# Performance work log

Hardware: AMD Instinct MI355X
Metric: run time of the kernel (lower is better)

Reference implementation:

```python
import jax, jax.numpy as jnp
import numpy as np

NUM_SPHERICAL = 7
NUM_RADIAL = 6
CUTOFF = 5.0
ENV_EXPONENT = 5
N_EDGES = 500000
N_TRIPLETS = 2000000


def _sph_jn_np(x, n):
    # spherical Bessel j_n(x) via upward recurrence (numpy, used for zero finding)
    j0 = np.sin(x) / x
    if n == 0:
        return j0
    j1 = np.sin(x) / x ** 2 - np.cos(x) / x
    jm1, j = j0, j1
    for l in range(1, n):
        jm1, j = j, (2 * l + 1) / x * j - jm1
    return j


def _jn_zeros(n, k):
    # zeros of spherical Bessel j_l, l=0..n-1, first k each (interlacing + bisection)
    def bisect(f, a, b):
        fa = f(a)
        for _ in range(80):
            m = 0.5 * (a + b)
            fm = f(m)
            if fa * fm <= 0:
                b = m
            else:
                a, fa = m, fm
        return 0.5 * (a + b)

    zerosj = np.zeros((n, k))
    zerosj[0] = np.arange(1, k + 1) * np.pi
    points = np.arange(1, k + n) * np.pi
    for i in range(1, n):
        m = k + n - 1 - i
        racines = np.zeros(m)
        for j in range(m):
            racines[j] = bisect(lambda r: _sph_jn_np(r, i), points[j], points[j + 1])
        points = racines
        zerosj[i] = racines[:k]
    return zerosj


_Z = _jn_zeros(NUM_SPHERICAL, NUM_RADIAL)  # [L, R] Bessel zeros
_BNORM = np.array([[1.0 / np.sqrt(0.5 * _sph_jn_np(_Z[l, n], l + 1) ** 2)
                    for n in range(NUM_RADIAL)] for l in range(NUM_SPHERICAL)])  # [L, R]
_YNORM = np.array([np.sqrt((2 * l + 1) / (4 * np.pi)) for l in range(NUM_SPHERICAL)])


def _sph_jn(x, n):
    # jnp spherical Bessel j_n via upward recurrence; x > 0 guaranteed here
    j0 = jnp.sin(x) / x
    if n == 0:
        return j0
    j1 = jnp.sin(x) / x ** 2 - jnp.cos(x) / x
    jm1, j = j0, j1
    for l in range(1, n):
        jm1, j = j, (2 * l + 1) / x * j - jm1
    return j


def setup_inputs() -> dict:
    key = jax.random.key(0)
    k1, k2, k3, k4 = jax.random.split(key, 4)
    D_ca = jax.random.uniform(k1, (N_EDGES,), dtype=jnp.float32) * (0.99 * CUTOFF) + 0.01
    Angle_cab = jax.random.uniform(k2, (N_TRIPLETS,), dtype=jnp.float32) * np.pi
    id3_reduce_ca = jax.random.randint(k3, (N_TRIPLETS,), 0, N_EDGES, dtype=jnp.int32)
    Kidx = jax.random.randint(k4, (N_TRIPLETS,), 0, 64, dtype=jnp.int32)
    return {"D_ca": D_ca, "Angle_cab": Angle_cab,
            "id3_reduce_ca": id3_reduce_ca, "Kidx": Kidx}


def reference(D_ca, Angle_cab, id3_reduce_ca, Kidx):
    L, R = NUM_SPHERICAL, NUM_RADIAL
    inv_cutoff = 1.0 / CUTOFF
    d = D_ca * inv_cutoff  # [E]

    # envelope u(d) = 1/d + a d^{p-1} + b d^p + c d^{p+1}, zero for d >= 1
    p = ENV_EXPONENT + 1
    a = -(p + 1) * (p + 2) / 2.0
    b = float(p * (p + 2))
    c = -p * (p + 1) / 2.0
    env = 1.0 / d + a * d ** (p - 1) + b * d ** p + c * d ** (p + 1)
    u_d = jnp.where(d < 1.0, env, jnp.zeros_like(d))

    zf = jnp.asarray(_Z, dtype=d.dtype)      # [L, R]
    bn = jnp.asarray(_BNORM, dtype=d.dtype)  # [L, R]
    # radial basis: norm_{l,n} * j_l(z_{l,n} * d)   -> [E, L, R]
    rbf = jnp.stack([bn[l] * _sph_jn(d[:, None] * zf[l], l) for l in range(L)], axis=1)
    norm_const = inv_cutoff ** 1.5
    rbf_env = (u_d * norm_const)[:, None, None] * rbf  # [E, L, R]

    # angular basis: Y_l^0(theta) = sqrt((2l+1)/4pi) * P_l(cos theta)  -> [T, L]
    ct = jnp.cos(Angle_cab)
    P = [jnp.ones_like(ct), ct]
    for l in range(1, L - 1):
        P.append(((2 * l + 1) * ct * P[l] - l * P[l - 1]) / (l + 1))
    yn = jnp.asarray(_YNORM, dtype=ct.dtype)
    sph = jnp.stack([yn[l] * P[l] for l in range(L)], axis=1)  # [T, L]

    # gather per-edge radial features to triplets and modulate by angular part
    out = rbf_env[id3_reduce_ca] * sph[:, :, None]  # [T, L, R]
    return out.reshape(-1, L * R)
```

## Files before the change

### kernel.cpp

```cpp
#include <hip/hip_runtime.h>
#include <math.h>
#include <stdint.h>

#define NSPH 7
#define NRAD 6
#define BLK  256
#define EPB  6
#define NE_PAD 48

typedef float f32x2 __attribute__((ext_vector_type(2)));
typedef float f32x4 __attribute__((ext_vector_type(4)));

#define SC_HPI_INV 0x1.45F306DC9C883p+23
#define SC_HPI     0x1.921FB54442D18p+0
#define SC_C0      (0x1p+0)
#define SC_C1      (-0x1.ffffffd0c621cp-2)
#define SC_C2      (0x1.55553e1068f19p-5)
#define SC_C3      (-0x1.6c087e89a359dp-10)
#define SC_C4      (0x1.99343027bf8c3p-16)
#define SC_S1      (-0x1.555545995a603p-3)
#define SC_S2      (0x1.1107605230bc4p-7)
#define SC_S3      (-0x1.994eb3774cf24p-13)

__device__ __forceinline__ unsigned abstop12(float x) {
    return (__float_as_uint(x) >> 20) & 0x7ffu;
}

__device__ __forceinline__ float sp_sin(double x, double x2) {
    double x3 = __dmul_rn(x, x2);
    double s1 = __dadd_rn(SC_S2, __dmul_rn(x2, SC_S3));
    double x7 = __dmul_rn(x3, x2);
    double s  = __dadd_rn(x, __dmul_rn(x3, SC_S1));
    return (float)__dadd_rn(s, __dmul_rn(x7, s1));
}

__device__ __forceinline__ float sp_cos(double x2, bool neg) {
    double c0 = neg ? -SC_C0 : SC_C0;
    double c1 = neg ? -SC_C1 : SC_C1;
    double c2 = neg ? -SC_C2 : SC_C2;
    double c3 = neg ? -SC_C3 : SC_C3;
    double c4 = neg ? -SC_C4 : SC_C4;
    double x4  = __dmul_rn(x2, x2);
    double c2v = __dadd_rn(c3, __dmul_rn(x2, c4));
    double c1v = __dadd_rn(c0, __dmul_rn(x2, c1));
    double x6  = __dmul_rn(x4, x2);
    double c   = __dadd_rn(c1v, __dmul_rn(x4, c2));
    return (float)__dadd_rn(c, __dmul_rn(x6, c2v));
}

__device__ __forceinline__ float sp_cos_pos(double x2) {
    double x4  = __dmul_rn(x2, x2);
    double c2v = __dadd_rn(SC_C3, __dmul_rn(x2, SC_C4));
    double c1v = __dadd_rn(SC_C0, __dmul_rn(x2, SC_C1));
    double x6  = __dmul_rn(x4, x2);
    double c   = __dadd_rn(c1v, __dmul_rn(x4, SC_C2));
    return (float)__dadd_rn(c, __dmul_rn(x6, c2v));
}

__device__ __forceinline__ double reduce_fast(double x, int* np) {
    double r = __dmul_rn(x, SC_HPI_INV);
    int n = (((int)r) + 0x800000) >> 24;
    *np = n;
    return __dsub_rn(x, __dmul_rn((double)n, SC_HPI));
}

__device__ __forceinline__ float glibc_cosf(float y) {
    unsigned at = abstop12(y);
    double x = (double)y;
    if (at < 0x3f4u) {
        if (at < 0x398u) return 1.0f;
        return sp_cos(__dmul_rn(x, x), false);
    }
    int n;
    double r = reduce_fast(x, &n);
    double s = ((n + 2) & 2) ? -1.0 : 1.0;
    bool neg = ((n + 1) & 2) != 0;
    int m = n ^ 1;
    double xs = __dmul_rn(r, s);
    double x2 = __dmul_rn(r, r);
    if ((m & 1) == 0) return sp_sin(xs, x2);
    return sp_cos(x2, neg);
}

__device__ __forceinline__ void glibc_sincosf(float y, float& so, float& co) {
    unsigned at = abstop12(y);
    double x = (double)y;
    if (at < 0x3f4u) {
        if (at < 0x398u) { so = y; co = 1.0f; return; }
        double x2 = __dmul_rn(x, x);
        so = sp_sin(x, x2);
        co = sp_cos(x2, false);
        return;
    }
    int n;
    double r = reduce_fast(x, &n);
    double x2 = __dmul_rn(r, r);
    double ss = ((n + 1) & 2) ? -1.0 : 1.0;
    double cs = ((n + 2) & 2) ? -1.0 : 1.0;
    bool sneg = (n & 2) != 0;
    bool cneg = ((n + 1) & 2) != 0;
    if ((n & 1) == 0) {
        so = sp_sin(__dmul_rn(r, ss), x2);
        co = sp_cos(x2, cneg);
    } else {
        so = sp_cos(x2, sneg);
        co = sp_sin(__dmul_rn(r, cs), x2);
    }
}

__device__ __forceinline__ void sincos_nr(float y, float& so, float& co) {
    int n;
    double r = reduce_fast((double)y, &n);
    double x2 = __dmul_rn(r, r);
    float sps = sp_sin(r, x2);
    float spc = sp_cos_pos(x2);
    unsigned sbit = (unsigned)(n & 2) << 30;
    unsigned cbit = (unsigned)((n + 1) & 2) << 30;
    bool odd = (n & 1) != 0;
    float sv = odd ? spc : sps;
    float cv = odd ? sps : spc;
    so = __uint_as_float(__float_as_uint(sv) ^ sbit);
    co = __uint_as_float(__float_as_uint(cv) ^ cbit);
}

__device__ __forceinline__ double jn_f64(double x, int n) {
    double s = sin(x), c = cos(x);
    double j0 = s / x;
    if (n == 0) return j0;
    double j1 = s / (x * x) - c / x;
    double jm1 = j0, j = j1;
    for (int l = 1; l < n; ++l) {
        double t = (double)(2 * l + 1) / x * j - jm1;
        jm1 = j; j = t;
    }
    return j;
}

__global__ __launch_bounds__(704) void setup_k(float* __restrict__ cst) {
    __shared__ double pts[13];
    __shared__ double roots[12];
    __shared__ double Z[NSPH][NRAD];
    const double PI = 3.141592653589793238462643383279502884;
    int tid = threadIdx.x, wv = tid >> 6, ln = tid & 63;
    if (tid < 12) pts[tid] = PI * (double)(tid + 1);
    __syncthreads();
    if (tid < NRAD) Z[0][tid] = pts[tid];
    for (int i = 1; i < NSPH; ++i) {
        int m = NRAD + NSPH - 1 - i;
        if (wv < m) {
            double a = pts[wv], b = pts[wv + 1];
            for (int r = 0; r < 9; ++r) {
                double st = (b - a) * (1.0 / 63.0);
                double f = jn_f64(a + st * (double)ln, i);
                double f0 = __shfl(f, 0);
                unsigned long long bm = __ballot((ln > 0) && (f0 * f <= 0.0));
                int idx = bm ? (__ffsll((unsigned long long)bm) - 1) : 63;
                b = a + st * (double)idx;
                a = a + st * (double)(idx - 1);
            }
            if (ln == 0) roots[wv] = 0.5 * (a + b);
        }
        __syncthreads();
        if (tid < m) pts[tid] = roots[tid];
        if (tid < NRAD) Z[i][tid] = roots[tid];
        __syncthreads();
    }
    if (tid < NSPH * NRAD) {
        int l = tid / NRAD;
        double z = Z[l][tid % NRAD];
        cst[tid] = (float)z;
        double jp = jn_f64(z, l + 1);
        cst[42 + tid] = (float)(1.0 / sqrt(0.5 * (jp * jp)));
    }
    if (tid < NSPH) {
        cst[84 + tid] = (float)sqrt((double)(2 * tid + 1) / (4.0 * PI));
    }
}

__global__ __launch_bounds__(252) void edge_k(
    const float* __restrict__ D, const float* __restrict__ cst,
    float* __restrict__ tab, int nE)
{
    __shared__ float zf[42], bn[42];
    __shared__ float sh_d[EPB], sh_unc[EPB];
    int tid = threadIdx.x;
    if (tid < 42) { zf[tid] = cst[tid]; bn[tid] = cst[42 + tid]; }
    int l   = tid / 36;
    int rem = tid - l * 36;
    int le  = rem / 6;
    int n   = rem - le * 6;
    int k   = l * 6 + n;
    long long e = (long long)blockIdx.x * EPB + le;
    bool ok = e < (long long)nE;
    if (ok && k == 0) {
        float d = __fmul_rn(D[e], 0.2f);
        float invd = __fdiv_rn(1.0f, d);
        float d2 = d * d, d4 = d2 * d2, d5 = d4 * d, d6 = d5 * d, d7 = d6 * d;
        float env = ((invd + (-28.0f) * d5) + 48.0f * d6) + (-21.0f) * d7;
        float u_d = (d < 1.0f) ? env : 0.0f;
        const float NC = (float)0.0894427190999916;
        sh_unc[le] = __fmul_rn(u_d, NC);
        sh_d[le] = d;
    }
    __syncthreads();
    if (!ok) return;
    float d = sh_d[le], unc = sh_unc[le];

    float x = __fmul_rn(d, zf[k]);
    float s, c;
    sincos_nr(x, s, c);
    float j = __fdiv_rn(s, x);
    if (l > 0) {
        float x2 = __fmul_rn(x, x);
        float j1 = __fsub_rn(__fdiv_rn(s, x2), __fdiv_rn(c, x));
        float jm1 = j, jc = j1;
        for (int kk = 1; kk < l; ++kk) {
            float fk = __fdiv_rn((float)(2 * kk + 1), x);
            float jn2 = __fsub_rn(__fmul_rn(fk, jc), jm1);
            jm1 = jc; jc = jn2;
        }
        j = jc;
    }
    tab[e * NE_PAD + k] = __fmul_rn(unc, __fmul_rn(bn[k], j));
}

__global__ __launch_bounds__(BLK) void trip_k(
    const float* __restrict__ Ang, const int* __restrict__ id3,
    const float* __restrict__ tab, const float* __restrict__ cst,
    float* __restrict__ out, int nT)
{
    __shared__ int   esh[BLK];
    __shared__ float ysh[BLK * 8];
    int tid = threadIdx.x;
    int base = blockIdx.x * BLK;
    int t = base + tid;
    bool ok = t < nT;
    int e = ok ? __builtin_nontemporal_load(id3 + t) : 0;
    float ang = ok ? __builtin_nontemporal_load(Ang + t) : 0.0f;
    esh[tid] = e * 24;

    float ct = glibc_cosf(ang);
    float P[NSPH];
    P[0] = 1.0f; P[1] = ct;
#pragma unroll
    for (int l = 1; l < NSPH - 1; ++l) {
        float t1 = __fmul_rn(__fmul_rn((float)(2 * l + 1), ct), P[l]);
        float t2 = __fmul_rn((float)l, P[l - 1]);
        P[l + 1] = __fdiv_rn(__fsub_rn(t1, t2), (float)(l + 1));
    }
#pragma unroll
    for (int l = 0; l < NSPH; ++l)
        ysh[tid * 8 + l] = __fmul_rn(cst[84 + l], P[l]);
    __syncthreads();

    const f32x2* tab2 = (const f32x2*)tab;
    f32x2* dst = (f32x2*)out + (long long)base * 21;
    int nv = nT - base; if (nv > BLK) nv = BLK;
    if (nv == BLK) {
#pragma unroll
        for (int it = 0; it < 21; ++it) {
            int i = tid + it * BLK;
            int r = i / 21, p = i - r * 21;
            f32x2 v = tab2[esh[r] + p];
            float ym = ysh[r * 8 + p / 3];
            f32x2 w;
            w.x = __fmul_rn(v.x, ym);
            w.y = __fmul_rn(v.y, ym);
            __builtin_nontemporal_store(w, dst + i);
        }
    } else {
        int nf2 = nv * 21; if (nf2 < 0) nf2 = 0;
        for (int i = tid; i < nf2; i += BLK) {
            int r = i / 21, p = i - r * 21;
            f32x2 v = tab2[esh[r] + p];
            float ym = ysh[r * 8 + p / 3];
            f32x2 w;
            w.x = __fmul_rn(v.x, ym);
            w.y = __fmul_rn(v.y, ym);
            __builtin_nontemporal_store(w, dst + i);
        }
    }
}

__global__ __launch_bounds__(BLK) void sph_main(
    const float* __restrict__ D, const float* __restrict__ Ang,
    const int* __restrict__ id3, const float* __restrict__ cst,
    float* __restrict__ out, int nT)
{
    __shared__ float zf[42], bn[42], yn[7];
    __shared__ float stg[BLK * 42];
    int tid = threadIdx.x;
    if (tid < 42) { zf[tid] = cst[tid]; bn[tid] = cst[42 + tid]; }
    if (tid < 7)  { yn[tid] = cst[84 + tid]; }
    __syncthreads();
    int base = blockIdx.x * BLK;
    int t = base + tid;
    bool ok = t < nT;
    int e = ok ? id3[t] : 0;
    float Dv = D[e];
    float ang = ok ? Ang[t] : 0.0f;
    float d = __fmul_rn(Dv, 0.2f);
    float invd = __fdiv_rn(1.0f, d);
    float d2 = d * d, d4 = d2 * d2, d5 = d4 * d, d6 = d5 * d, d7 = d6 * d;
    float env = ((invd + (-28.0f) * d5) + 48.0f * d6) + (-21.0f) * d7;
    float u_d = (d < 1.0f) ? env : 0.0f;
    const float NC = (float)0.0894427190999916;
    float unc = __fmul_rn(u_d, NC);
    float ct = glibc_cosf(ang);
    float P[NSPH];
    P[0] = 1.0f; P[1] = ct;
#pragma unroll
    for (int l = 1; l < NSPH - 1; ++l) {
        float t1 = __fmul_rn(__fmul_rn((float)(2 * l + 1), ct), P[l]);
        float t2 = __fmul_rn((float)l, P[l - 1]);
        P[l + 1] = __fdiv_rn(__fsub_rn(t1, t2), (float)(l + 1));
    }
    float* row = &stg[tid * 42];
#pragma unroll
    for (int l = 0; l < NSPH; ++l) {
        float yPl = __fmul_rn(yn[l], P[l]);
        for (int n = 0; n < NRAD; ++n) {
            float z = zf[l * 6 + n];
            float x = __fmul_rn(d, z);
            float s, c;
            glibc_sincosf(x, s, c);
            float j = __fdiv_rn(s, x);
            if (l > 0) {
                float x2 = __fmul_rn(x, x);
                float j1 = __fsub_rn(__fdiv_rn(s, x2), __fdiv_rn(c, x));
                float jm1 = j, jc = j1;
                for (int kk = 1; kk < l; ++kk) {
                    float fk = __fdiv_rn((float)(2 * kk + 1), x);
                    float jn2 = __fsub_rn(__fmul_rn(fk, jc), jm1);
                    jm1 = jc; jc = jn2;
                }
                j = jc;
            }
            float re = __fmul_rn(unc, __fmul_rn(bn[l * 6 + n], j));
            row[l * 6 + n] = __fmul_rn(re, yPl);
        }
    }
    __syncthreads();
    int nv = nT - base; if (nv > BLK) nv = BLK;
    int nf2 = nv * 21;
    const float2* src = (const float2*)stg;
    float2* dst = (float2*)(out + (long long)base * 42);
    for (int i = tid; i < nf2; i += BLK) dst[i] = src[i];
}

extern "C" void kernel_launch(void* const* d_in, const int* in_sizes, int n_in,
                              void* d_out, int out_size, void* d_ws, size_t ws_size,
                              hipStream_t stream) {
    const float* D   = (const float*)d_in[0];
    const float* Ang = (const float*)d_in[1];
    const int*   id3 = (const int*)d_in[2];
    float* out = (float*)d_out;
    int nE = in_sizes[0];
    int nT = in_sizes[1];

    size_t tab_bytes = (size_t)nE * NE_PAD * sizeof(float);
    if (ws_size >= tab_bytes + 512) {
        float* tab = (float*)d_ws;
        float* cst = (float*)((char*)d_ws + tab_bytes);
        setup_k<<<1, 704, 0, stream>>>(cst);
        int gA = (nE + EPB - 1) / EPB;
        edge_k<<<gA, 252, 0, stream>>>(D, cst, tab, nE);
        int gB = (nT + BLK - 1) / BLK;
        trip_k<<<gB, BLK, 0, stream>>>(Ang, id3, tab, cst, out, nT);
    } else {
        float* cst = (float*)d_ws;
        setup_k<<<1, 704, 0, stream>>>(cst);
        int grid = (nT + BLK - 1) / BLK;
        sph_main<<<grid, BLK, 0, stream>>>(D, Ang, id3, cst, out, nT);
    }
}
```

Before: 264.6 us.

## Split envelope into separate kernel and remap edge_k threads per wavefront by l

The envelope computation moves out of edge_k into a new env_k kernel that writes the per-edge scale into padding slot 47 of the table, which removes the shared-memory staging and the __syncthreads in edge_k. edge_k now uses 448-thread blocks with one 64-lane wavefront per spherical order l, so each wavefront runs the same Bessel recurrence length and divergence drops. The cost is an extra kernel launch, an extra table read per thread, and 4 idle lanes per wavefront.

```diff
diff --git a/kernel.cpp b/kernel.cpp
--- a/kernel.cpp
+++ b/kernel.cpp
@@ -5,7 +5,7 @@
 #define NSPH 7
 #define NRAD 6
 #define BLK  256
-#define EPB  6
+#define EPB2 10
 #define NE_PAD 48
 
 typedef float f32x2 __attribute__((ext_vector_type(2)));
@@ -177,36 +177,39 @@
     }
 }
 
-__global__ __launch_bounds__(252) void edge_k(
+__global__ __launch_bounds__(BLK) void env_k(
+    const float* __restrict__ D, float* __restrict__ tab, int nE)
+{
+    int e = blockIdx.x * BLK + threadIdx.x;
+    if (e >= nE) return;
+    float d = __fmul_rn(D[e], 0.2f);
+    float invd = __fdiv_rn(1.0f, d);
+    float d2 = d * d, d4 = d2 * d2, d5 = d4 * d, d6 = d5 * d, d7 = d6 * d;
+    float env = ((invd + (-28.0f) * d5) + 48.0f * d6) + (-21.0f) * d7;
+    float u_d = (d < 1.0f) ? env : 0.0f;
+    const float NC = (float)0.0894427190999916;
+    tab[(long long)e * NE_PAD + 47] = __fmul_rn(u_d, NC);
+}
+
+__global__ __launch_bounds__(448) void edge_k(
     const float* __restrict__ D, const float* __restrict__ cst,
     float* __restrict__ tab, int nE)
 {
-    __shared__ float zf[42], bn[42];
-    __shared__ float sh_d[EPB], sh_unc[EPB];
     int tid = threadIdx.x;
-    if (tid < 42) { zf[tid] = cst[tid]; bn[tid] = cst[42 + tid]; }
-    int l   = tid / 36;
-    int rem = tid - l * 36;
-    int le  = rem / 6;
-    int n   = rem - le * 6;
-    int k   = l * 6 + n;
-    long long e = (long long)blockIdx.x * EPB + le;
-    bool ok = e < (long long)nE;
-    if (ok && k == 0) {
-        float d = __fmul_rn(D[e], 0.2f);
-        float invd = __fdiv_rn(1.0f, d);
-        float d2 = d * d, d4 = d2 * d2, d5 = d4 * d, d6 = d5 * d, d7 = d6 * d;
-        float env = ((invd + (-28.0f) * d5) + 48.0f * d6) + (-21.0f) * d7;
-        float u_d = (d < 1.0f) ? env : 0.0f;
-        const float NC = (float)0.0894427190999916;
-        sh_unc[le] = __fmul_rn(u_d, NC);
-        sh_d[le] = d;
-    }
-    __syncthreads();
-    if (!ok) return;
-    float d = sh_d[le], unc = sh_unc[le];
-
-    float x = __fmul_rn(d, zf[k]);
+    int l    = tid >> 6;
+    int ln   = tid & 63;
+    int slot = ln / 6;
+    int n    = ln - slot * 6;
+    long long e = (long long)blockIdx.x * EPB2 + slot;
+    if (slot >= EPB2 || e >= (long long)nE) return;
+    int k = l * 6 + n;
+
+    float d   = __fmul_rn(D[e], 0.2f);
+    float unc = tab[e * NE_PAD + 47];
+    float z   = cst[k];
+    float bnk = cst[42 + k];
+
+    float x = __fmul_rn(d, z);
     float s, c;
     sincos_nr(x, s, c);
     float j = __fdiv_rn(s, x);
@@ -221,7 +224,7 @@
         }
         j = jc;
     }
-    tab[e * NE_PAD + k] = __fmul_rn(unc, __fmul_rn(bn[k], j));
+    tab[e * NE_PAD + k] = __fmul_rn(unc, __fmul_rn(bnk, j));
 }
 
 __global__ __launch_bounds__(BLK) void trip_k(
@@ -363,8 +366,9 @@
         float* tab = (float*)d_ws;
         float* cst = (float*)((char*)d_ws + tab_bytes);
         setup_k<<<1, 704, 0, stream>>>(cst);
-        int gA = (nE + EPB - 1) / EPB;
-        edge_k<<<gA, 252, 0, stream>>>(D, cst, tab, nE);
+        env_k<<<(nE + BLK - 1) / BLK, BLK, 0, stream>>>(D, tab, nE);
+        int gA = (nE + EPB2 - 1) / EPB2;
+        edge_k<<<gA, 448, 0, stream>>>(D, cst, tab, nE);
         int gB = (nT + BLK - 1) / BLK;
         trip_k<<<gB, BLK, 0, stream>>>(Ang, id3, tab, cst, out, nT);
     } else {
```

Result: no change. 264.3 us (-0.1%).
